# Kernel optimization log

Measured on AMD Instinct MI355X. Metric: run time of the kernel, lower is better.

Reference implementation:

```python
import jax, jax.numpy as jnp
import numpy as np

D = 256          # input_size
RNN = 256        # rnn_hidden
COND = 64        # cond_dim
HID = 128        # MLP hidden
N_FIXED = 128    # mask.sum() with alternating mask
N_FREE = D - N_FIXED
B = 131072

# Static index arrays implementing the boolean mask (even indices fixed).
IDX_FIXED = np.arange(0, D, 2)
IDX_FREE = np.arange(1, D, 2)


def setup_inputs() -> dict:
    key = jax.random.key(0)
    ks = jax.random.split(key, 8)
    in_dim = N_FIXED + RNN + COND  # 448
    x = jax.random.normal(ks[0], (B, D), jnp.float32)
    h = jax.random.normal(ks[1], (B, RNN + COND), jnp.float32)
    W1 = jax.random.normal(ks[2], (in_dim, HID), jnp.float32) / np.sqrt(in_dim)
    b1 = jnp.zeros((HID,), jnp.float32)
    W2 = jax.random.normal(ks[3], (HID, HID), jnp.float32) / np.sqrt(HID)
    b2 = jnp.zeros((HID,), jnp.float32)
    W3 = jax.random.normal(ks[4], (HID, N_FREE * 2), jnp.float32) / np.sqrt(HID)
    b3 = jnp.zeros((N_FREE * 2,), jnp.float32)
    return {"x": x, "h": h, "W1": W1, "b1": b1, "W2": W2, "b2": b2, "W3": W3, "b3": b3}


def reference(x, h, W1, b1, W2, b2, W3, b3):
    # gather fixed / free halves (static index gather == boolean-mask select)
    x_fixed = x[:, IDX_FIXED]          # [B, N_FIXED]
    x_free = x[:, IDX_FREE]            # [B, N_FREE]
    z = jnp.concatenate([x_fixed, h], axis=-1)  # [B, 448]
    a = jax.nn.relu(z @ W1 + b1)
    a = jax.nn.relu(a @ W2 + b2)
    st = a @ W3 + b3                   # [B, 2*N_FREE]
    s = jnp.tanh(st[:, :N_FREE])
    t = st[:, N_FREE:]
    y_free = x_free * jnp.exp(s) + t
    log_det = jnp.sum(s, axis=-1)
    # scatter-write back into output layout
    y = jnp.zeros_like(x).at[:, IDX_FIXED].set(x_fixed).at[:, IDX_FREE].set(y_free)
    return y, log_det
```

## Files before the change

### kernel.cpp

```cpp
#include <hip/hip_runtime.h>
#include <hip/hip_bf16.h>
#include <stdint.h>

typedef __attribute__((ext_vector_type(8))) short bf16x8;
typedef __attribute__((ext_vector_type(4))) float f32x4;

#define B_ROWS 131072
#define BM 16
#define XP 268
#define ZHP 328
#define AP 136

#define XS_BYTES (BM * XP * 4)
#define ZH_OFF   XS_BYTES
#define ZH_BYTES (BM * ZHP * 2)
#define A1_OFF   (ZH_OFF + ZH_BYTES)
#define A1_BYTES (BM * AP * 2)
#define LSUM_OFF (A1_OFF + A1_BYTES)
#define LDS_TOTAL (LSUM_OFF + 64 * 4)

#define W1P_OFF 0
#define W2P_OFF 7168
#define W3P_OFF 9216

__device__ inline uint16_t f2bf(float x) {
  uint32_t u = __float_as_uint(x);
  u += 0x7fffu + ((u >> 16) & 1u);
  return (uint16_t)(u >> 16);
}

__device__ inline float tanh_fast(float x) {
  x = fminf(fmaxf(x, -15.f), 15.f);
  float e = __expf(2.f * x);
  return (e - 1.f) / (e + 1.f);
}

__global__ void prepack_kernel(const float* __restrict__ W1,
                               const float* __restrict__ W2,
                               const float* __restrict__ W3,
                               uint4* __restrict__ wp) {
  int tid = blockIdx.x * 256 + threadIdx.x;
  if (tid >= 13312) return;
  int l = tid & 63, f = tid >> 6;
  const float* W; int N, kt, nt;
  if (f < 112)      { W = W1; N = 128; int ff = f;       nt = ff / 14; kt = ff - nt * 14; }
  else if (f < 144) { W = W2; N = 128; int ff = f - 112; nt = ff >> 2; kt = ff & 3; }
  else              { W = W3; N = 256; int ff = f - 144; nt = ff >> 2; kt = ff & 3; }
  int k0  = kt * 32 + (l >> 4) * 8;
  int col = nt * 16 + (l & 15);
  uint16_t v[8];
#pragma unroll
  for (int j = 0; j < 8; j++) v[j] = f2bf(W[(size_t)(k0 + j) * N + col]);
  uint4 o;
  o.x = (uint32_t)v[0] | ((uint32_t)v[1] << 16);
  o.y = (uint32_t)v[2] | ((uint32_t)v[3] << 16);
  o.z = (uint32_t)v[4] | ((uint32_t)v[5] << 16);
  o.w = (uint32_t)v[6] | ((uint32_t)v[7] << 16);
  wp[tid] = o;
}

__global__ __launch_bounds__(256, 5) void fused_kernel(
    const float* __restrict__ x, const float* __restrict__ h,
    const float* __restrict__ b1, const float* __restrict__ b2,
    const float* __restrict__ b3, const uint4* __restrict__ wp,
    float* __restrict__ y, float* __restrict__ ldet) {
  extern __shared__ uint8_t smem[];
  float*    xs   = (float*)smem;
  uint16_t* zh   = (uint16_t*)(smem + ZH_OFF);
  uint16_t* a1   = (uint16_t*)(smem + A1_OFF);
  uint16_t* a2   = zh;
  float*    lsum = (float*)(smem + LSUM_OFF);

  const int t  = threadIdx.x;
  const int m0 = blockIdx.x * BM;

  {
    const float4* xg = (const float4*)(x + (size_t)m0 * 256);
#pragma unroll
    for (int k = 0; k < 4; k++) {
      int idx = t + k * 256;
      int row = idx >> 6, c4 = idx & 63;
      *(float4*)&xs[row * XP + c4 * 4] = xg[idx];
    }
    const float4* hg = (const float4*)(h + (size_t)m0 * 320);
#pragma unroll
    for (int k = 0; k < 5; k++) {
      int idx = t + k * 256;
      int row = idx / 80, c4 = idx - row * 80;
      float4 v = hg[idx];
      uint2 p;
      p.x = (uint32_t)f2bf(v.x) | ((uint32_t)f2bf(v.y) << 16);
      p.y = (uint32_t)f2bf(v.z) | ((uint32_t)f2bf(v.w) << 16);
      *(uint2*)&zh[row * ZHP + c4 * 4] = p;
    }
  }
  __syncthreads();

  const int wid = t >> 6, l = t & 63;
  const int lr = l & 15, lq = l >> 4;

  {
    f32x4 acc[2] = {};
#pragma unroll
    for (int kt = 0; kt < 4; kt++) {
      int base = lr * XP + kt * 64 + lq * 16;
      float4 q0 = *(const float4*)&xs[base + 0];
      float4 q1 = *(const float4*)&xs[base + 4];
      float4 q2 = *(const float4*)&xs[base + 8];
      float4 q3 = *(const float4*)&xs[base + 12];
      union { bf16x8 v; __hip_bfloat162 h2[4]; } u;
      u.h2[0] = __float22bfloat162_rn(make_float2(q0.x, q0.z));
      u.h2[1] = __float22bfloat162_rn(make_float2(q1.x, q1.z));
      u.h2[2] = __float22bfloat162_rn(make_float2(q2.x, q2.z));
      u.h2[3] = __float22bfloat162_rn(make_float2(q3.x, q3.z));
      bf16x8 bfr0 = *(const bf16x8*)&wp[W1P_OFF + ((wid * 2 + 0) * 14 + kt) * 64 + l];
      bf16x8 bfr1 = *(const bf16x8*)&wp[W1P_OFF + ((wid * 2 + 1) * 14 + kt) * 64 + l];
      acc[0] = __builtin_amdgcn_mfma_f32_16x16x32_bf16(u.v, bfr0, acc[0], 0, 0, 0);
      acc[1] = __builtin_amdgcn_mfma_f32_16x16x32_bf16(u.v, bfr1, acc[1], 0, 0, 0);
    }
#pragma unroll 2
    for (int kt = 4; kt < 14; kt++) {
      bf16x8 afr = *(const bf16x8*)&zh[lr * ZHP + (kt - 4) * 32 + lq * 8];
      bf16x8 bfr0 = *(const bf16x8*)&wp[W1P_OFF + ((wid * 2 + 0) * 14 + kt) * 64 + l];
      bf16x8 bfr1 = *(const bf16x8*)&wp[W1P_OFF + ((wid * 2 + 1) * 14 + kt) * 64 + l];
      acc[0] = __builtin_amdgcn_mfma_f32_16x16x32_bf16(afr, bfr0, acc[0], 0, 0, 0);
      acc[1] = __builtin_amdgcn_mfma_f32_16x16x32_bf16(afr, bfr1, acc[1], 0, 0, 0);
    }
#pragma unroll
    for (int nj = 0; nj < 2; nj++) {
      int col = wid * 32 + nj * 16 + lr;
      float bv = b1[col];
#pragma unroll
      for (int r = 0; r < 4; r++)
        a1[(lq * 4 + r) * AP + col] = f2bf(fmaxf(acc[nj][r] + bv, 0.f));
    }
  }
  __syncthreads();

  {
    f32x4 acc[2] = {};
#pragma unroll
    for (int kt = 0; kt < 4; kt++) {
      bf16x8 afr = *(const bf16x8*)&a1[lr * AP + kt * 32 + lq * 8];
      bf16x8 bfr0 = *(const bf16x8*)&wp[W2P_OFF + ((wid * 2 + 0) * 4 + kt) * 64 + l];
      bf16x8 bfr1 = *(const bf16x8*)&wp[W2P_OFF + ((wid * 2 + 1) * 4 + kt) * 64 + l];
      acc[0] = __builtin_amdgcn_mfma_f32_16x16x32_bf16(afr, bfr0, acc[0], 0, 0, 0);
      acc[1] = __builtin_amdgcn_mfma_f32_16x16x32_bf16(afr, bfr1, acc[1], 0, 0, 0);
    }
#pragma unroll
    for (int nj = 0; nj < 2; nj++) {
      int col = wid * 32 + nj * 16 + lr;
      float bv = b2[col];
#pragma unroll
      for (int r = 0; r < 4; r++)
        a2[(lq * 4 + r) * AP + col] = f2bf(fmaxf(acc[nj][r] + bv, 0.f));
    }
  }
  __syncthreads();

  f32x4 acc3[4] = {};
#pragma unroll
  for (int kt = 0; kt < 4; kt++) {
    bf16x8 afr = *(const bf16x8*)&a2[lr * AP + kt * 32 + lq * 8];
    bf16x8 bfrS0 = *(const bf16x8*)&wp[W3P_OFF + ((wid * 2 + 0) * 4 + kt) * 64 + l];
    bf16x8 bfrS1 = *(const bf16x8*)&wp[W3P_OFF + ((wid * 2 + 1) * 4 + kt) * 64 + l];
    bf16x8 bfrT0 = *(const bf16x8*)&wp[W3P_OFF + ((8 + wid * 2 + 0) * 4 + kt) * 64 + l];
    bf16x8 bfrT1 = *(const bf16x8*)&wp[W3P_OFF + ((8 + wid * 2 + 1) * 4 + kt) * 64 + l];
    acc3[0] = __builtin_amdgcn_mfma_f32_16x16x32_bf16(afr, bfrS0, acc3[0], 0, 0, 0);
    acc3[1] = __builtin_amdgcn_mfma_f32_16x16x32_bf16(afr, bfrS1, acc3[1], 0, 0, 0);
    acc3[2] = __builtin_amdgcn_mfma_f32_16x16x32_bf16(afr, bfrT0, acc3[2], 0, 0, 0);
    acc3[3] = __builtin_amdgcn_mfma_f32_16x16x32_bf16(afr, bfrT1, acc3[3], 0, 0, 0);
  }

  float lp[4] = {0.f, 0.f, 0.f, 0.f};
#pragma unroll
  for (int nj = 0; nj < 2; nj++) {
    int colc = wid * 32 + nj * 16 + lr;
    float bs = b3[colc];
    float bt = b3[128 + colc];
#pragma unroll
    for (int r = 0; r < 4; r++) {
      int lrow = lq * 4 + r;
      float sv = tanh_fast(acc3[nj][r] + bs);
      float tv = acc3[nj + 2][r] + bt;
      lp[r] += sv;
      const float2 xv = *(const float2*)&xs[lrow * XP + 2 * colc];
      float2 o;
      o.x = xv.x;
      o.y = xv.y * __expf(sv) + tv;
      *(float2*)(y + (size_t)(m0 + lrow) * 256 + 2 * colc) = o;
    }
  }

#pragma unroll
  for (int r = 0; r < 4; r++) {
    float v = lp[r];
    v += __shfl_xor(v, 1);
    v += __shfl_xor(v, 2);
    v += __shfl_xor(v, 4);
    v += __shfl_xor(v, 8);
    if (lr == 0) lsum[wid * BM + lq * 4 + r] = v;
  }
  __syncthreads();
  if (t < BM)
    ldet[m0 + t] = lsum[t] + lsum[BM + t] + lsum[2 * BM + t] + lsum[3 * BM + t];
}

extern "C" void kernel_launch(void* const* d_in, const int* in_sizes, int n_in,
                              void* d_out, int out_size, void* d_ws, size_t ws_size,
                              hipStream_t stream) {
  const float* x  = (const float*)d_in[0];
  const float* h  = (const float*)d_in[1];
  const float* W1 = (const float*)d_in[2];
  const float* b1 = (const float*)d_in[3];
  const float* W2 = (const float*)d_in[4];
  const float* b2 = (const float*)d_in[5];
  const float* W3 = (const float*)d_in[6];
  const float* b3 = (const float*)d_in[7];
  float* y    = (float*)d_out;
  float* ldet = y + (size_t)B_ROWS * 256;
  uint4* wp   = (uint4*)d_ws;

  prepack_kernel<<<52, 256, 0, stream>>>(W1, W2, W3, wp);

  (void)hipFuncSetAttribute((const void*)fused_kernel,
                            hipFuncAttributeMaxDynamicSharedMemorySize, LDS_TOTAL);
  fused_kernel<<<B_ROWS / BM, 256, LDS_TOTAL, stream>>>(x, h, b1, b2, b3, wp, y, ldet);
}
```

Baseline: 127.1 us.

## Make fused kernel persistent with double-buffered async global-to-LDS prefetch

Converts the one-tile-per-block kernel into a persistent kernel of 512 blocks, each looping over 16 row tiles. The next tile's x and h are prefetched with global_load_lds directly into a second LDS buffer while the current tile is computed. An XOR swizzle on the LDS layout replaces padding to avoid bank conflicts. The h-to-bf16 conversion moves from load time to fragment read. This aims to overlap HBM loads with MFMA work, at the cost of more LDS per block, lower occupancy (launch bounds 2), and fewer blocks in flight.

Result: slower. 131.1 us (+3.1%).

```diff
diff --git a/kernel.cpp b/kernel.cpp
--- a/kernel.cpp
+++ b/kernel.cpp
@@ -7,21 +7,27 @@
 
 #define B_ROWS 131072
 #define BM 16
-#define XP 268
-#define ZHP 328
+#define NT 16
+#define GRID 512
+
+#define XB 16384
+#define HB 20480
+#define H_OFF 32768
+#define A1_OFF 73728
+#define LSUM_OFF 78080
+#define LDS_TOTAL 78336
 #define AP 136
-
-#define XS_BYTES (BM * XP * 4)
-#define ZH_OFF   XS_BYTES
-#define ZH_BYTES (BM * ZHP * 2)
-#define A1_OFF   (ZH_OFF + ZH_BYTES)
-#define A1_BYTES (BM * AP * 2)
-#define LSUM_OFF (A1_OFF + A1_BYTES)
-#define LDS_TOTAL (LSUM_OFF + 64 * 4)
 
 #define W1P_OFF 0
 #define W2P_OFF 7168
 #define W3P_OFF 9216
+
+typedef const __attribute__((address_space(1))) unsigned int gu32;
+typedef __attribute__((address_space(3))) unsigned int lu32;
+
+__device__ inline void gl_lds16(const void* g, void* l) {
+  __builtin_amdgcn_global_load_lds((gu32*)g, (lu32*)l, 16, 0, 0);
+}
 
 __device__ inline uint16_t f2bf(float x) {
   uint32_t u = __float_as_uint(x);
@@ -59,151 +65,184 @@
   wp[tid] = o;
 }
 
-__global__ __launch_bounds__(256, 5) void fused_kernel(
+__global__ __launch_bounds__(256, 2) void fused_kernel(
     const float* __restrict__ x, const float* __restrict__ h,
     const float* __restrict__ b1, const float* __restrict__ b2,
     const float* __restrict__ b3, const uint4* __restrict__ wp,
     float* __restrict__ y, float* __restrict__ ldet) {
   extern __shared__ uint8_t smem[];
-  float*    xs   = (float*)smem;
-  uint16_t* zh   = (uint16_t*)(smem + ZH_OFF);
   uint16_t* a1   = (uint16_t*)(smem + A1_OFF);
-  uint16_t* a2   = zh;
   float*    lsum = (float*)(smem + LSUM_OFF);
 
-  const int t  = threadIdx.x;
-  const int m0 = blockIdx.x * BM;
-
-  {
-    const float4* xg = (const float4*)(x + (size_t)m0 * 256);
-#pragma unroll
-    for (int k = 0; k < 4; k++) {
-      int idx = t + k * 256;
-      int row = idx >> 6, c4 = idx & 63;
-      *(float4*)&xs[row * XP + c4 * 4] = xg[idx];
-    }
-    const float4* hg = (const float4*)(h + (size_t)m0 * 320);
-#pragma unroll
-    for (int k = 0; k < 5; k++) {
-      int idx = t + k * 256;
-      int row = idx / 80, c4 = idx - row * 80;
-      float4 v = hg[idx];
-      uint2 p;
-      p.x = (uint32_t)f2bf(v.x) | ((uint32_t)f2bf(v.y) << 16);
-      p.y = (uint32_t)f2bf(v.z) | ((uint32_t)f2bf(v.w) << 16);
-      *(uint2*)&zh[row * ZHP + c4 * 4] = p;
-    }
-  }
-  __syncthreads();
-
+  const int t = threadIdx.x;
   const int wid = t >> 6, l = t & 63;
   const int lr = l & 15, lq = l >> 4;
+  const int tile0 = blockIdx.x * NT;
+
+  int xoff[4], hoff[5];
+#pragma unroll
+  for (int k = 0; k < 4; k++) {
+    int r = wid * 4 + k;
+    int c = (l & ~15) | ((l & 15) ^ (r & 15));
+    xoff[k] = r * 256 + c * 4;
+  }
+#pragma unroll
+  for (int k = 0; k < 5; k++) {
+    int s = (wid * 5 + k) * 64 + l;
+    int r = s / 80, cp = s - r * 80;
+    int c = (cp & ~15) | ((cp & 15) ^ (r & 15));
+    hoff[k] = r * 320 + c * 4;
+  }
 
   {
-    f32x4 acc[2] = {};
+    const float* xg = x + (size_t)(tile0 * BM) * 256;
+    const float* hg = h + (size_t)(tile0 * BM) * 320;
+#pragma unroll
+    for (int k = 0; k < 4; k++)
+      gl_lds16(xg + xoff[k], smem + (wid * 4 + k) * 1024);
+#pragma unroll
+    for (int k = 0; k < 5; k++)
+      gl_lds16(hg + hoff[k], smem + H_OFF + (wid * 5 + k) * 1024);
+  }
+
+  int cur = 0;
+  for (int it = 0; it < NT; ++it) {
+    const int m0 = (tile0 + it) * BM;
+    __syncthreads();
+
+    const uint8_t* xsc = smem + cur * XB;
+    const uint8_t* hsc = smem + H_OFF + cur * HB;
+    uint16_t* a2 = (uint16_t*)(smem + H_OFF + cur * HB);
+
+    if (it + 1 < NT) {
+      const float* xg = x + (size_t)(m0 + BM) * 256;
+      const float* hg = h + (size_t)(m0 + BM) * 320;
+      uint8_t* xd = smem + (cur ^ 1) * XB;
+      uint8_t* hd = smem + H_OFF + (cur ^ 1) * HB;
+#pragma unroll
+      for (int k = 0; k < 4; k++)
+        gl_lds16(xg + xoff[k], xd + (wid * 4 + k) * 1024);
+#pragma unroll
+      for (int k = 0; k < 5; k++)
+        gl_lds16(hg + hoff[k], hd + (wid * 5 + k) * 1024);
+    }
+
+    {
+      f32x4 acc[2] = {};
+#pragma unroll
+      for (int kt = 0; kt < 4; kt++) {
+        union { bf16x8 v; __hip_bfloat162 h2[4]; } u;
+#pragma unroll
+        for (int i = 0; i < 4; i++) {
+          int slot = kt * 16 + ((lq * 4 + i) ^ lr);
+          float4 q = *(const float4*)(xsc + lr * 1024 + slot * 16);
+          u.h2[i] = __float22bfloat162_rn(make_float2(q.x, q.z));
+        }
+        bf16x8 bfr0 = *(const bf16x8*)&wp[W1P_OFF + ((wid * 2 + 0) * 14 + kt) * 64 + l];
+        bf16x8 bfr1 = *(const bf16x8*)&wp[W1P_OFF + ((wid * 2 + 1) * 14 + kt) * 64 + l];
+        acc[0] = __builtin_amdgcn_mfma_f32_16x16x32_bf16(u.v, bfr0, acc[0], 0, 0, 0);
+        acc[1] = __builtin_amdgcn_mfma_f32_16x16x32_bf16(u.v, bfr1, acc[1], 0, 0, 0);
+      }
+#pragma unroll 2
+      for (int kh = 0; kh < 10; kh++) {
+        int c0 = kh * 8 + lq * 2;
+        int qd = c0 & ~15, mm = c0 & 15;
+        float4 a = *(const float4*)(hsc + lr * 1280 + (qd | (mm ^ lr)) * 16);
+        float4 b = *(const float4*)(hsc + lr * 1280 + (qd | ((mm + 1) ^ lr)) * 16);
+        union { bf16x8 v; __hip_bfloat162 h2[4]; } u;
+        u.h2[0] = __float22bfloat162_rn(make_float2(a.x, a.y));
+        u.h2[1] = __float22bfloat162_rn(make_float2(a.z, a.w));
+        u.h2[2] = __float22bfloat162_rn(make_float2(b.x, b.y));
+        u.h2[3] = __float22bfloat162_rn(make_float2(b.z, b.w));
+        int kt = kh + 4;
+        bf16x8 bfr0 = *(const bf16x8*)&wp[W1P_OFF + ((wid * 2 + 0) * 14 + kt) * 64 + l];
+        bf16x8 bfr1 = *(const bf16x8*)&wp[W1P_OFF + ((wid * 2 + 1) * 14 + kt) * 64 + l];
+        acc[0] = __builtin_amdgcn_mfma_f32_16x16x32_bf16(u.v, bfr0, acc[0], 0, 0, 0);
+        acc[1] = __builtin_amdgcn_mfma_f32_16x16x32_bf16(u.v, bfr1, acc[1], 0, 0, 0);
+      }
+#pragma unroll
+      for (int nj = 0; nj < 2; nj++) {
+        int col = wid * 32 + nj * 16 + lr;
+        float bv = b1[col];
+#pragma unroll
+        for (int r = 0; r < 4; r++)
+          a1[(lq * 4 + r) * AP + col] = f2bf(fmaxf(acc[nj][r] + bv, 0.f));
+      }
+    }
+    __syncthreads();
+
+    {
+      f32x4 acc[2] = {};
+#pragma unroll
+      for (int kt = 0; kt < 4; kt++) {
+        bf16x8 afr = *(const bf16x8*)&a1[lr * AP + kt * 32 + lq * 8];
+        bf16x8 bfr0 = *(const bf16x8*)&wp[W2P_OFF + ((wid * 2 + 0) * 4 + kt) * 64 + l];
+        bf16x8 bfr1 = *(const bf16x8*)&wp[W2P_OFF + ((wid * 2 + 1) * 4 + kt) * 64 + l];
+        acc[0] = __builtin_amdgcn_mfma_f32_16x16x32_bf16(afr, bfr0, acc[0], 0, 0, 0);
+        acc[1] = __builtin_amdgcn_mfma_f32_16x16x32_bf16(afr, bfr1, acc[1], 0, 0, 0);
+      }
+#pragma unroll
+      for (int nj = 0; nj < 2; nj++) {
+        int col = wid * 32 + nj * 16 + lr;
+        float bv = b2[col];
+#pragma unroll
+        for (int r = 0; r < 4; r++)
+          a2[(lq * 4 + r) * AP + col] = f2bf(fmaxf(acc[nj][r] + bv, 0.f));
+      }
+    }
+    __syncthreads();
+
+    f32x4 acc3[4] = {};
 #pragma unroll
     for (int kt = 0; kt < 4; kt++) {
-      int base = lr * XP + kt * 64 + lq * 16;
-      float4 q0 = *(const float4*)&xs[base + 0];
-      float4 q1 = *(const float4*)&xs[base + 4];
-      float4 q2 = *(const float4*)&xs[base + 8];
-      float4 q3 = *(const float4*)&xs[base + 12];
-      union { bf16x8 v; __hip_bfloat162 h2[4]; } u;
-      u.h2[0] = __float22bfloat162_rn(make_float2(q0.x, q0.z));
-      u.h2[1] = __float22bfloat162_rn(make_float2(q1.x, q1.z));
-      u.h2[2] = __float22bfloat162_rn(make_float2(q2.x, q2.z));
-      u.h2[3] = __float22bfloat162_rn(make_float2(q3.x, q3.z));
-      bf16x8 bfr0 = *(const bf16x8*)&wp[W1P_OFF + ((wid * 2 + 0) * 14 + kt) * 64 + l];
-      bf16x8 bfr1 = *(const bf16x8*)&wp[W1P_OFF + ((wid * 2 + 1) * 14 + kt) * 64 + l];
-      acc[0] = __builtin_amdgcn_mfma_f32_16x16x32_bf16(u.v, bfr0, acc[0], 0, 0, 0);
-      acc[1] = __builtin_amdgcn_mfma_f32_16x16x32_bf16(u.v, bfr1, acc[1], 0, 0, 0);
-    }
-#pragma unroll 2
-    for (int kt = 4; kt < 14; kt++) {
-      bf16x8 afr = *(const bf16x8*)&zh[lr * ZHP + (kt - 4) * 32 + lq * 8];
-      bf16x8 bfr0 = *(const bf16x8*)&wp[W1P_OFF + ((wid * 2 + 0) * 14 + kt) * 64 + l];
-      bf16x8 bfr1 = *(const bf16x8*)&wp[W1P_OFF + ((wid * 2 + 1) * 14 + kt) * 64 + l];
-      acc[0] = __builtin_amdgcn_mfma_f32_16x16x32_bf16(afr, bfr0, acc[0], 0, 0, 0);
-      acc[1] = __builtin_amdgcn_mfma_f32_16x16x32_bf16(afr, bfr1, acc[1], 0, 0, 0);
-    }
+      bf16x8 afr = *(const bf16x8*)&a2[lr * AP + kt * 32 + lq * 8];
+      bf16x8 bfrS0 = *(const bf16x8*)&wp[W3P_OFF + ((wid * 2 + 0) * 4 + kt) * 64 + l];
+      bf16x8 bfrS1 = *(const bf16x8*)&wp[W3P_OFF + ((wid * 2 + 1) * 4 + kt) * 64 + l];
+      bf16x8 bfrT0 = *(const bf16x8*)&wp[W3P_OFF + ((8 + wid * 2 + 0) * 4 + kt) * 64 + l];
+      bf16x8 bfrT1 = *(const bf16x8*)&wp[W3P_OFF + ((8 + wid * 2 + 1) * 4 + kt) * 64 + l];
+      acc3[0] = __builtin_amdgcn_mfma_f32_16x16x32_bf16(afr, bfrS0, acc3[0], 0, 0, 0);
+      acc3[1] = __builtin_amdgcn_mfma_f32_16x16x32_bf16(afr, bfrS1, acc3[1], 0, 0, 0);
+      acc3[2] = __builtin_amdgcn_mfma_f32_16x16x32_bf16(afr, bfrT0, acc3[2], 0, 0, 0);
+      acc3[3] = __builtin_amdgcn_mfma_f32_16x16x32_bf16(afr, bfrT1, acc3[3], 0, 0, 0);
+    }
+
+    float lp[4] = {0.f, 0.f, 0.f, 0.f};
 #pragma unroll
     for (int nj = 0; nj < 2; nj++) {
-      int col = wid * 32 + nj * 16 + lr;
-      float bv = b1[col];
-#pragma unroll
-      for (int r = 0; r < 4; r++)
-        a1[(lq * 4 + r) * AP + col] = f2bf(fmaxf(acc[nj][r] + bv, 0.f));
-    }
-  }
-  __syncthreads();
-
-  {
-    f32x4 acc[2] = {};
-#pragma unroll
-    for (int kt = 0; kt < 4; kt++) {
-      bf16x8 afr = *(const bf16x8*)&a1[lr * AP + kt * 32 + lq * 8];
-      bf16x8 bfr0 = *(const bf16x8*)&wp[W2P_OFF + ((wid * 2 + 0) * 4 + kt) * 64 + l];
-      bf16x8 bfr1 = *(const bf16x8*)&wp[W2P_OFF + ((wid * 2 + 1) * 4 + kt) * 64 + l];
-      acc[0] = __builtin_amdgcn_mfma_f32_16x16x32_bf16(afr, bfr0, acc[0], 0, 0, 0);
-      acc[1] = __builtin_amdgcn_mfma_f32_16x16x32_bf16(afr, bfr1, acc[1], 0, 0, 0);
-    }
-#pragma unroll
-    for (int nj = 0; nj < 2; nj++) {
-      int col = wid * 32 + nj * 16 + lr;
-      float bv = b2[col];
-#pragma unroll
-      for (int r = 0; r < 4; r++)
-        a2[(lq * 4 + r) * AP + col] = f2bf(fmaxf(acc[nj][r] + bv, 0.f));
-    }
-  }
-  __syncthreads();
-
-  f32x4 acc3[4] = {};
-#pragma unroll
-  for (int kt = 0; kt < 4; kt++) {
-    bf16x8 afr = *(const bf16x8*)&a2[lr * AP + kt * 32 + lq * 8];
-    bf16x8 bfrS0 = *(const bf16x8*)&wp[W3P_OFF + ((wid * 2 + 0) * 4 + kt) * 64 + l];
-    bf16x8 bfrS1 = *(const bf16x8*)&wp[W3P_OFF + ((wid * 2 + 1) * 4 + kt) * 64 + l];
-    bf16x8 bfrT0 = *(const bf16x8*)&wp[W3P_OFF + ((8 + wid * 2 + 0) * 4 + kt) * 64 + l];
-    bf16x8 bfrT1 = *(const bf16x8*)&wp[W3P_OFF + ((8 + wid * 2 + 1) * 4 + kt) * 64 + l];
-    acc3[0] = __builtin_amdgcn_mfma_f32_16x16x32_bf16(afr, bfrS0, acc3[0], 0, 0, 0);
-    acc3[1] = __builtin_amdgcn_mfma_f32_16x16x32_bf16(afr, bfrS1, acc3[1], 0, 0, 0);
-    acc3[2] = __builtin_amdgcn_mfma_f32_16x16x32_bf16(afr, bfrT0, acc3[2], 0, 0, 0);
-    acc3[3] = __builtin_amdgcn_mfma_f32_16x16x32_bf16(afr, bfrT1, acc3[3], 0, 0, 0);
-  }
-
-  float lp[4] = {0.f, 0.f, 0.f, 0.f};
-#pragma unroll
-  for (int nj = 0; nj < 2; nj++) {
-    int colc = wid * 32 + nj * 16 + lr;
-    float bs = b3[colc];
-    float bt = b3[128 + colc];
+      int colc = wid * 32 + nj * 16 + lr;
+      float bs = b3[colc];
+      float bt = b3[128 + colc];
+#pragma unroll
+      for (int r = 0; r < 4; r++) {
+        int lrow = lq * 4 + r;
+        float sv = tanh_fast(acc3[nj][r] + bs);
+        float tv = acc3[nj + 2][r] + bt;
+        lp[r] += sv;
+        int cch = wid * 16 + nj * 8 + (lr >> 1);
+        int slot = (cch & ~15) | ((cch & 15) ^ lrow);
+        const float2 xv = *(const float2*)(xsc + lrow * 1024 + slot * 16 + (lr & 1) * 8);
+        float2 o;
+        o.x = xv.x;
+        o.y = xv.y * __expf(sv) + tv;
+        *(float2*)(y + (size_t)(m0 + lrow) * 256 + 2 * colc) = o;
+      }
+    }
+
 #pragma unroll
     for (int r = 0; r < 4; r++) {
-      int lrow = lq * 4 + r;
-      float sv = tanh_fast(acc3[nj][r] + bs);
-      float tv = acc3[nj + 2][r] + bt;
-      lp[r] += sv;
-      const float2 xv = *(const float2*)&xs[lrow * XP + 2 * colc];
-      float2 o;
-      o.x = xv.x;
-      o.y = xv.y * __expf(sv) + tv;
-      *(float2*)(y + (size_t)(m0 + lrow) * 256 + 2 * colc) = o;
-    }
-  }
-
-#pragma unroll
-  for (int r = 0; r < 4; r++) {
-    float v = lp[r];
-    v += __shfl_xor(v, 1);
-    v += __shfl_xor(v, 2);
-    v += __shfl_xor(v, 4);
-    v += __shfl_xor(v, 8);
-    if (lr == 0) lsum[wid * BM + lq * 4 + r] = v;
-  }
-  __syncthreads();
-  if (t < BM)
-    ldet[m0 + t] = lsum[t] + lsum[BM + t] + lsum[2 * BM + t] + lsum[3 * BM + t];
+      float v = lp[r];
+      v += __shfl_xor(v, 1);
+      v += __shfl_xor(v, 2);
+      v += __shfl_xor(v, 4);
+      v += __shfl_xor(v, 8);
+      if (lr == 0) lsum[wid * BM + lq * 4 + r] = v;
+    }
+    __syncthreads();
+    if (t < BM)
+      ldet[m0 + t] = lsum[t] + lsum[BM + t] + lsum[2 * BM + t] + lsum[3 * BM + t];
+
+    cur ^= 1;
+  }
 }
 
 extern "C" void kernel_launch(void* const* d_in, const int* in_sizes, int n_in,
@@ -225,5 +264,5 @@
 
   (void)hipFuncSetAttribute((const void*)fused_kernel,
                             hipFuncAttributeMaxDynamicSharedMemorySize, LDS_TOTAL);
-  fused_kernel<<<B_ROWS / BM, 256, LDS_TOTAL, stream>>>(x, h, b1, b2, b3, wp, y, ldet);
-}
+  fused_kernel<<<GRID, 256, LDS_TOTAL, stream>>>(x, h, b1, b2, b3, wp, y, ldet);
+}
```
